# Performance work log

Hardware: AMD Instinct MI355X
Metric: run time of the kernel (lower is better)

The kernel has to match this reference:

```python
import jax, jax.numpy as jnp
import numpy as np

V, E, U, B, T = 50000, 256, 512, 256, 256  # vocab, embed, units, batch, seq_len


def setup_inputs() -> dict:
    key = jax.random.key(0)
    ks = jax.random.split(key, 10)
    tokens = jax.random.randint(ks[0], (B, T), 0, V)
    emb = jax.random.normal(ks[1], (V, E), dtype=jnp.float32) * 0.02
    s_e = 1.0 / np.sqrt(E)
    s_u = 1.0 / np.sqrt(U)
    W0 = jax.random.normal(ks[2], (E, 4 * U), dtype=jnp.float32) * s_e
    U0 = jax.random.normal(ks[3], (U, 4 * U), dtype=jnp.float32) * s_u
    b0 = jnp.zeros((4 * U,), dtype=jnp.float32)
    W1 = jax.random.normal(ks[4], (U, 4 * U), dtype=jnp.float32) * s_u
    U1 = jax.random.normal(ks[5], (U, 4 * U), dtype=jnp.float32) * s_u
    b1 = jnp.zeros((4 * U,), dtype=jnp.float32)
    Wd = jax.random.normal(ks[6], (U, 1), dtype=jnp.float32) * s_u
    bd = jnp.zeros((1,), dtype=jnp.float32)
    return {"tokens": tokens, "emb": emb, "W0": W0, "U0": U0, "b0": b0,
            "W1": W1, "U1": U1, "b1": b1, "Wd": Wd, "bd": bd}


def _lstm_gates(z, c):
    # Keras gate order: i, f, g (candidate), o
    i, f, g, o = jnp.split(z, 4, axis=-1)
    c_new = jax.nn.sigmoid(f) * c + jax.nn.sigmoid(i) * jnp.tanh(g)
    h_new = jax.nn.sigmoid(o) * jnp.tanh(c_new)
    return h_new, c_new


def reference(tokens, emb, W0, U0, b0, W1, U1, b1, Wd, bd):
    x = emb[tokens]  # [B, T, E]
    # Precompute input projections for layer 0 in one big GEMM: [T, B, 4U]
    xz0 = jnp.einsum('bte,ef->tbf', x, W0) + b0

    h0 = jnp.zeros((tokens.shape[0], U0.shape[0]), dtype=x.dtype)
    c0 = jnp.zeros_like(h0)
    h1 = jnp.zeros_like(h0)
    c1 = jnp.zeros_like(h0)

    def step(carry, xz_t):
        h0, c0, h1, c1 = carry
        h0, c0 = _lstm_gates(xz_t + h0 @ U0, c0)
        h1, c1 = _lstm_gates(h0 @ W1 + h1 @ U1 + b1, c1)
        return (h0, c0, h1, c1), None

    (h0, c0, h1, c1), _ = jax.lax.scan(step, (h0, c0, h1, c1), xz0)
    return jax.nn.sigmoid(h1 @ Wd + bd)  # [B, 1]
```

## Files before the change

### kernel.cpp

```cpp
#include <hip/hip_runtime.h>
#include <hip/hip_bf16.h>
#include <math.h>

#define VB 50000
#define EE 256
#define UU 512
#define BB 256
#define TT 256
#define G4 2048

typedef __attribute__((ext_vector_type(8))) short short8;
typedef __attribute__((ext_vector_type(2))) unsigned long long u64x2;
typedef __attribute__((ext_vector_type(4))) float f32x4;

__device__ __forceinline__ float sigf(float x){ return 1.0f/(1.0f+expf(-x)); }
__device__ __forceinline__ unsigned short f2bf(float f){
    __hip_bfloat16 h = __float2bfloat16(f);
    unsigned short s; __builtin_memcpy(&s,&h,2); return s;
}
__device__ __forceinline__ float bf2f(unsigned short u){
    unsigned int x = ((unsigned int)u)<<16; float f; __builtin_memcpy(&f,&x,4); return f;
}

__device__ __forceinline__ unsigned int cldu(const unsigned int* p){
    return __hip_atomic_load(p, __ATOMIC_RELAXED, __HIP_MEMORY_SCOPE_AGENT);
}
__device__ __forceinline__ void cstu(unsigned int* p, unsigned int v){
    __hip_atomic_store(p, v, __ATOMIC_RELAXED, __HIP_MEMORY_SCOPE_AGENT);
}

__device__ __forceinline__ short8 cld16w(const unsigned short* p){
    short8 v;
    asm volatile("global_load_dwordx4 %0, %1, off sc1"
                 : "=&v"(v) : "v"(p));
    return v;
}
__device__ __forceinline__ void cst16w(unsigned long long* dp, u64x2 v){
    asm volatile("global_store_dwordx4 %0, %1, off sc1"
                 :: "v"(dp), "v"(v) : "memory");
}

__global__ __launch_bounds__(256) void wtrans(const float* __restrict__ in, int rows,
                                              unsigned short* __restrict__ out,
                                              int Kout, int koff) {
    __shared__ float tl[32][33];
    int tx = threadIdx.x, ty = threadIdx.y;
    int c0 = blockIdx.x * 32, k0 = blockIdx.y * 32;
    #pragma unroll
    for (int i = 0; i < 4; i++)
        tl[ty + i * 8][tx] = in[(size_t)(k0 + ty + i * 8) * G4 + c0 + tx];
    __syncthreads();
    #pragma unroll
    for (int i = 0; i < 4; i++)
        out[(size_t)(c0 + ty + i * 8) * Kout + koff + k0 + tx] = f2bf(tl[tx][ty + i * 8]);
}

__global__ __launch_bounds__(64) void xgather(const int* __restrict__ tokens,
                                              const float* __restrict__ emb,
                                              unsigned short* __restrict__ xbf) {
    int flat = blockIdx.x;
    int b = flat & 255, t = flat >> 8;
    int tok = tokens[b * TT + t];
    float4 v = ((const float4*)(emb + (size_t)tok * EE))[threadIdx.x];
    ushort4 o;
    o.x = f2bf(v.x); o.y = f2bf(v.y); o.z = f2bf(v.z); o.w = f2bf(v.w);
    ((ushort4*)(xbf + ((size_t)t * BB + b) * EE))[threadIdx.x] = o;
}

__global__ __launch_bounds__(256, 1) void rnn_persist(
    const unsigned short* __restrict__ Wt0,
    const unsigned short* __restrict__ Wt1,
    const unsigned short* __restrict__ xbf,
    const int* __restrict__ tokens, const float* __restrict__ emb,
    const float* __restrict__ b0v, const float* __restrict__ b1v,
    unsigned short* __restrict__ h0buf,
    unsigned short* __restrict__ h1buf,
    unsigned int* __restrict__ bars,
    int use_xbf)
{
    extern __shared__ char smem[];
    unsigned short* wl  = (unsigned short*)smem;
    unsigned short* hst = (unsigned short*)(smem + 131072);
    int*            tokl = (int*)(smem + 131072 + 3072);

    const int tid   = threadIdx.x;
    const int bid   = blockIdx.x;
    const int g     = bid >> 6;
    const int local = bid & 63;
    const int layer = local >> 5;
    const int u0    = (local & 31) * 16;
    const int row0  = g * 64;
    const int K     = layer ? 1024 : 768;
    const int KT    = K / 32;
    const unsigned short* Wt = layer ? Wt1 : Wt0;
    const float* bR = layer ? b1v : b0v;

    const int nch = 4 * KT * 64;
    for (int i = tid; i < nch; i += 256) {
        int n  = i & 15;
        int q2 = (i >> 4) & 3;
        int t2 = i >> 6;
        int kt = t2 % KT, gate = t2 / KT;
        const unsigned short* src = Wt + (size_t)(gate * UU + u0 + n) * K + kt * 32 + q2 * 8;
        *(short8*)(wl + (size_t)i * 8) = *(const short8*)src;
    }

    float gb[4];
    #pragma unroll
    for (int gate = 0; gate < 4; gate++) gb[gate] = bR[gate * UU + u0 + (tid & 15)];
    float cst[4] = {0.f, 0.f, 0.f, 0.f};

    const int lane = tid & 63;
    const int w    = tid >> 6;
    const int n16  = lane & 15;
    const int q    = lane >> 4;
    const int q8   = q * 8;
    const int myrow = row0 + w * 16 + n16;
    const unsigned short* wlane = wl + lane * 8;

    unsigned int* flg = bars + (size_t)g * 1024;
    unsigned int* myFlag = flg + local;
    const unsigned int* pollp = flg + lane;
    const int pollSlack = (layer == 0 && lane >= 32) ? 6 : 0;

    const size_t HS = (size_t)BB * UU;

    __syncthreads();

    for (int p = 0; p <= TT; p++) {
        const bool active = layer ? (p >= 1) : (p < TT);

        f32x4 acc[4];
        #pragma unroll
        for (int gate = 0; gate < 4; gate++)
            acc[gate] = (f32x4){gb[gate], gb[gate], gb[gate], gb[gate]};

        short8 xv[8];
        if (layer == 0 && p < TT) {
            if (!use_xbf) {
                if (tid < 64) tokl[tid] = tokens[(size_t)(row0 + tid) * TT + p];
                __syncthreads();
                const float* ep = emb + (size_t)tokl[w * 16 + n16] * EE + q8;
                #pragma unroll
                for (int kt = 0; kt < 8; kt++) {
                    float4 f0 = *(const float4*)(ep + kt * 32);
                    float4 f1 = *(const float4*)(ep + kt * 32 + 4);
                    union { unsigned short s[8]; short8 v; } u;
                    u.s[0]=f2bf(f0.x); u.s[1]=f2bf(f0.y); u.s[2]=f2bf(f0.z); u.s[3]=f2bf(f0.w);
                    u.s[4]=f2bf(f1.x); u.s[5]=f2bf(f1.y); u.s[6]=f2bf(f1.z); u.s[7]=f2bf(f1.w);
                    #pragma unroll
                    for (int gate = 0; gate < 4; gate++) {
                        short8 bv = *(const short8*)(wlane + (size_t)(gate * KT + kt) * 512);
                        acc[gate] = __builtin_amdgcn_mfma_f32_16x16x32_bf16(u.v, bv, acc[gate], 0, 0, 0);
                    }
                }
            } else {
                const unsigned short* xp = xbf + ((size_t)p * BB + myrow) * EE + q8;
                #pragma unroll
                for (int kt = 0; kt < 8; kt++)
                    xv[kt] = *(const short8*)(xp + kt * 32);
            }
        }

        if (layer == 0) {
            if (p < TT) {
                if (tid < 64) {
                    const int thr = p - pollSlack;
                    for (;;) {
                        bool bad = ((int)cldu(pollp) < thr);
                        if (__ballot(bad) == 0ULL) break;
                        __builtin_amdgcn_s_sleep(1);
                    }
                }
                __syncthreads();

                const unsigned short* h0r = h0buf + (size_t)(p & 7) * HS;
                unsigned short* hw = h0buf + (size_t)((p + 1) & 7) * HS;
                const unsigned short* ah = h0r + (size_t)myrow * UU + q8;
                short8 hb[16];
                #pragma unroll
                for (int i = 0; i < 16; i++) hb[i] = cld16w(ah + i * 32);
                if (use_xbf) {
                    #pragma unroll
                    for (int kt = 0; kt < 8; kt++) {
                        #pragma unroll
                        for (int gate = 0; gate < 4; gate++) {
                            short8 bv = *(const short8*)(wlane + (size_t)(gate * KT + kt) * 512);
                            acc[gate] = __builtin_amdgcn_mfma_f32_16x16x32_bf16(xv[kt], bv, acc[gate], 0, 0, 0);
                        }
                    }
                }
                asm volatile("s_waitcnt vmcnt(0)" ::: "memory");
                __builtin_amdgcn_sched_barrier(0);
                #pragma unroll
                for (int i = 0; i < 16; i++) {
                    #pragma unroll
                    for (int gate = 0; gate < 4; gate++) {
                        short8 bv = *(const short8*)(wlane + (size_t)(gate * KT + 8 + i) * 512);
                        acc[gate] = __builtin_amdgcn_mfma_f32_16x16x32_bf16(hb[i], bv, acc[gate], 0, 0, 0);
                    }
                }

                #pragma unroll
                for (int r = 0; r < 4; r++) {
                    float zi = acc[0][r];
                    float zf = acc[1][r];
                    float zg = acc[2][r];
                    float zo = acc[3][r];
                    float cn = sigf(zf) * cst[r] + sigf(zi) * tanhf(zg);
                    cst[r] = cn;
                    hst[(w * 16 + q * 4 + r) * 24 + n16] = f2bf(sigf(zo) * tanhf(cn));
                }
                __syncthreads();
                if (tid < 128) {
                    int row = tid >> 1, half = tid & 1;
                    u64x2 sv = *(const u64x2*)(hst + row * 24 + half * 8);
                    unsigned long long* dp = (unsigned long long*)
                        (hw + (size_t)(row0 + row) * UU + u0 + half * 8);
                    cst16w(dp, sv);
                }
            }
        } else {
            if (active) {
                const unsigned short* h0r = h0buf + (size_t)(p & 7) * HS;
                const unsigned short* h1r = h1buf + (size_t)((p + 1) & 1) * HS;
                unsigned short* hw = h1buf + (size_t)(p & 1) * HS;
                const unsigned short* a0 = h0r + (size_t)myrow * UU + q8;
                const unsigned short* a1 = h1r + (size_t)myrow * UU + q8;

                for (;;) {
                    bool bad = (lane < 32) && ((int)cldu(pollp) < p);
                    if (__ballot(bad) == 0ULL) break;
                    __builtin_amdgcn_s_sleep(1);
                }
                short8 ha[16];
                #pragma unroll
                for (int i = 0; i < 16; i++) ha[i] = cld16w(a0 + i * 32);

                for (;;) {
                    bool bad = (lane >= 32) && ((int)cldu(pollp) < p);
                    if (__ballot(bad) == 0ULL) break;
                    __builtin_amdgcn_s_sleep(1);
                }
                short8 hc[16];
                #pragma unroll
                for (int i = 0; i < 16; i++) hc[i] = cld16w(a1 + i * 32);

                asm volatile("s_waitcnt vmcnt(16)" ::: "memory");
                __builtin_amdgcn_sched_barrier(0);
                #pragma unroll
                for (int i = 0; i < 16; i++) {
                    #pragma unroll
                    for (int gate = 0; gate < 4; gate++) {
                        short8 bv = *(const short8*)(wlane + (size_t)(gate * KT + i) * 512);
                        acc[gate] = __builtin_amdgcn_mfma_f32_16x16x32_bf16(ha[i], bv, acc[gate], 0, 0, 0);
                    }
                }
                asm volatile("s_waitcnt vmcnt(0)" ::: "memory");
                __builtin_amdgcn_sched_barrier(0);
                #pragma unroll
                for (int i = 0; i < 16; i++) {
                    #pragma unroll
                    for (int gate = 0; gate < 4; gate++) {
                        short8 bv = *(const short8*)(wlane + (size_t)(gate * KT + 16 + i) * 512);
                        acc[gate] = __builtin_amdgcn_mfma_f32_16x16x32_bf16(hc[i], bv, acc[gate], 0, 0, 0);
                    }
                }

                #pragma unroll
                for (int r = 0; r < 4; r++) {
                    float zi = acc[0][r];
                    float zf = acc[1][r];
                    float zg = acc[2][r];
                    float zo = acc[3][r];
                    float cn = sigf(zf) * cst[r] + sigf(zi) * tanhf(zg);
                    cst[r] = cn;
                    hst[(w * 16 + q * 4 + r) * 24 + n16] = f2bf(sigf(zo) * tanhf(cn));
                }
                __syncthreads();
                if (tid < 128) {
                    int row = tid >> 1, half = tid & 1;
                    u64x2 sv = *(const u64x2*)(hst + row * 24 + half * 8);
                    unsigned long long* dp = (unsigned long long*)
                        (hw + (size_t)(row0 + row) * UU + u0 + half * 8);
                    cst16w(dp, sv);
                }
            }
        }

        if (p < TT) {
            asm volatile("s_waitcnt vmcnt(0)" ::: "memory");
            __syncthreads();
            if (tid == 0) cstu(myFlag, (unsigned int)(p + 1));
        }
    }
}

__global__ __launch_bounds__(64) void dense_out(
    const unsigned short* __restrict__ h, const float* __restrict__ Wd,
    const float* __restrict__ bd, float* __restrict__ out)
{
    int b = blockIdx.x;
    int lane = threadIdx.x;
    float s = 0.f;
    #pragma unroll
    for (int k = lane; k < UU; k += 64) s += bf2f(h[(size_t)b * UU + k]) * Wd[k];
    #pragma unroll
    for (int off = 32; off > 0; off >>= 1) s += __shfl_down(s, off);
    if (lane == 0) out[b] = sigf(s + bd[0]);
}

extern "C" void kernel_launch(void* const* d_in, const int* in_sizes, int n_in,
                              void* d_out, int out_size, void* d_ws, size_t ws_size,
                              hipStream_t stream) {
    const int*   tokens = (const int*)  d_in[0];
    const float* emb    = (const float*)d_in[1];
    const float* W0     = (const float*)d_in[2];
    const float* U0     = (const float*)d_in[3];
    const float* b0     = (const float*)d_in[4];
    const float* W1     = (const float*)d_in[5];
    const float* U1     = (const float*)d_in[6];
    const float* b1     = (const float*)d_in[7];
    const float* Wd     = (const float*)d_in[8];
    const float* bd     = (const float*)d_in[9];
    float* out = (float*)d_out;

    const size_t oWt0 = 0;
    const size_t oWt1 = (size_t)G4 * 768 * 2;
    const size_t oH0  = oWt1 + (size_t)G4 * 1024 * 2;
    const size_t oH1  = oH0 + (size_t)8 * BB * UU * 2;
    const size_t oBar = oH1 + (size_t)2 * BB * UU * 2;
    const size_t oX   = oBar + 32768;
    const size_t needFull = oX + (size_t)TT * BB * EE * 2;
    int use_xbf = (ws_size >= needFull) ? 1 : 0;

    unsigned short* Wt0p = (unsigned short*)((char*)d_ws + oWt0);
    unsigned short* Wt1p = (unsigned short*)((char*)d_ws + oWt1);
    unsigned short* h0p  = (unsigned short*)((char*)d_ws + oH0);
    unsigned short* h1p  = (unsigned short*)((char*)d_ws + oH1);
    unsigned int*   barp = (unsigned int*)  ((char*)d_ws + oBar);
    unsigned short* xbfp = (unsigned short*)((char*)d_ws + oX);

    hipMemsetAsync((char*)d_ws + oH0, 0, oX - oH0, stream);

    wtrans<<<dim3(G4 / 32, EE / 32), dim3(32, 8), 0, stream>>>(W0, EE, Wt0p, 768, 0);
    wtrans<<<dim3(G4 / 32, UU / 32), dim3(32, 8), 0, stream>>>(U0, UU, Wt0p, 768, 256);
    wtrans<<<dim3(G4 / 32, UU / 32), dim3(32, 8), 0, stream>>>(W1, UU, Wt1p, 1024, 0);
    wtrans<<<dim3(G4 / 32, UU / 32), dim3(32, 8), 0, stream>>>(U1, UU, Wt1p, 1024, 512);

    if (use_xbf)
        xgather<<<dim3(BB * TT), dim3(64), 0, stream>>>(tokens, emb, xbfp);

    {
        const size_t shmem = 131072 + 3072 + 256;
        hipFuncSetAttribute((const void*)rnn_persist,
                            hipFuncAttributeMaxDynamicSharedMemorySize, (int)shmem);
        void* args[] = {(void*)&Wt0p, (void*)&Wt1p, (void*)&xbfp,
                        (void*)&tokens, (void*)&emb, (void*)&b0, (void*)&b1,
                        (void*)&h0p, (void*)&h1p, (void*)&barp, (void*)&use_xbf};
        hipLaunchCooperativeKernel((const void*)rnn_persist, dim3(256), dim3(256),
                                   args, shmem, stream);
    }

    dense_out<<<dim3(BB), dim3(64), 0, stream>>>(h1p, Wd, bd, out);
}
```

Before: 1.978 ms.

## Deepen hidden-state ring buffers and replace sc1 loads with periodic acquire fences

Grows the h0 and h1 ring buffers to 16 slots each. Hidden-state loads now go through the normal cached path instead of sc1, and an agent-scope acquire fence every 8 steps is meant to invalidate stale cached copies. The layer-0 wait on layer-1 progress moves from before the compute to just before the h0 store, so the compute overlaps that wait. Only slot 0 and the flag area are zeroed now, not the whole buffer region. The scheme depends on the 16-slot ring being deep enough that a reused slot's cached lines are never read stale between fences, which is a subtle correctness risk.

```diff
diff --git a/kernel.cpp b/kernel.cpp
--- a/kernel.cpp
+++ b/kernel.cpp
@@ -29,9 +29,9 @@
     __hip_atomic_store(p, v, __ATOMIC_RELAXED, __HIP_MEMORY_SCOPE_AGENT);
 }
 
-__device__ __forceinline__ short8 cld16w(const unsigned short* p){
+__device__ __forceinline__ short8 cld16c(const unsigned short* p){
     short8 v;
-    asm volatile("global_load_dwordx4 %0, %1, off sc1"
+    asm volatile("global_load_dwordx4 %0, %1, off"
                  : "=&v"(v) : "v"(p));
     return v;
 }
@@ -121,14 +121,14 @@
     unsigned int* flg = bars + (size_t)g * 1024;
     unsigned int* myFlag = flg + local;
     const unsigned int* pollp = flg + lane;
-    const int pollSlack = (layer == 0 && lane >= 32) ? 6 : 0;
 
     const size_t HS = (size_t)BB * UU;
 
     __syncthreads();
 
     for (int p = 0; p <= TT; p++) {
-        const bool active = layer ? (p >= 1) : (p < TT);
+        if ((p & 7) == 0)
+            __builtin_amdgcn_fence(__ATOMIC_ACQUIRE, "agent");
 
         f32x4 acc[4];
         #pragma unroll
@@ -165,21 +165,20 @@
         if (layer == 0) {
             if (p < TT) {
                 if (tid < 64) {
-                    const int thr = p - pollSlack;
                     for (;;) {
-                        bool bad = ((int)cldu(pollp) < thr);
+                        bool bad = (lane < 32) && ((int)cldu(pollp) < p);
                         if (__ballot(bad) == 0ULL) break;
                         __builtin_amdgcn_s_sleep(1);
                     }
                 }
                 __syncthreads();
 
-                const unsigned short* h0r = h0buf + (size_t)(p & 7) * HS;
-                unsigned short* hw = h0buf + (size_t)((p + 1) & 7) * HS;
+                const unsigned short* h0r = h0buf + (size_t)(p & 15) * HS;
+                unsigned short* hw = h0buf + (size_t)((p + 1) & 15) * HS;
                 const unsigned short* ah = h0r + (size_t)myrow * UU + q8;
                 short8 hb[16];
                 #pragma unroll
-                for (int i = 0; i < 16; i++) hb[i] = cld16w(ah + i * 32);
+                for (int i = 0; i < 16; i++) hb[i] = cld16c(ah + i * 32);
                 if (use_xbf) {
                     #pragma unroll
                     for (int kt = 0; kt < 8; kt++) {
@@ -212,6 +211,17 @@
                     hst[(w * 16 + q * 4 + r) * 24 + n16] = f2bf(sigf(zo) * tanhf(cn));
                 }
                 __syncthreads();
+
+                {
+                    const int thr = p - 6;
+                    if (thr > 0) {
+                        for (;;) {
+                            bool bad = (lane >= 32) && ((int)cldu(pollp) < thr);
+                            if (__ballot(bad) == 0ULL) break;
+                            __builtin_amdgcn_s_sleep(1);
+                        }
+                    }
+                }
                 if (tid < 128) {
                     int row = tid >> 1, half = tid & 1;
                     u64x2 sv = *(const u64x2*)(hst + row * 24 + half * 8);
@@ -221,10 +231,10 @@
                 }
             }
         } else {
-            if (active) {
-                const unsigned short* h0r = h0buf + (size_t)(p & 7) * HS;
-                const unsigned short* h1r = h1buf + (size_t)((p + 1) & 1) * HS;
-                unsigned short* hw = h1buf + (size_t)(p & 1) * HS;
+            if (p >= 1) {
+                const unsigned short* h0r = h0buf + (size_t)(p & 15) * HS;
+                const unsigned short* h1r = h1buf + (size_t)((p - 1) & 15) * HS;
+                unsigned short* hw = h1buf + (size_t)(p & 15) * HS;
                 const unsigned short* a0 = h0r + (size_t)myrow * UU + q8;
                 const unsigned short* a1 = h1r + (size_t)myrow * UU + q8;
 
@@ -235,7 +245,7 @@
                 }
                 short8 ha[16];
                 #pragma unroll
-                for (int i = 0; i < 16; i++) ha[i] = cld16w(a0 + i * 32);
+                for (int i = 0; i < 16; i++) ha[i] = cld16c(a0 + i * 32);
 
                 for (;;) {
                     bool bad = (lane >= 32) && ((int)cldu(pollp) < p);
@@ -244,7 +254,7 @@
                 }
                 short8 hc[16];
                 #pragma unroll
-                for (int i = 0; i < 16; i++) hc[i] = cld16w(a1 + i * 32);
+                for (int i = 0; i < 16; i++) hc[i] = cld16c(a1 + i * 32);
 
                 asm volatile("s_waitcnt vmcnt(16)" ::: "memory");
                 __builtin_amdgcn_sched_barrier(0);
@@ -325,11 +335,12 @@
     const float* bd     = (const float*)d_in[9];
     float* out = (float*)d_out;
 
+    const size_t SLOT = (size_t)BB * UU * 2;
     const size_t oWt0 = 0;
     const size_t oWt1 = (size_t)G4 * 768 * 2;
     const size_t oH0  = oWt1 + (size_t)G4 * 1024 * 2;
-    const size_t oH1  = oH0 + (size_t)8 * BB * UU * 2;
-    const size_t oBar = oH1 + (size_t)2 * BB * UU * 2;
+    const size_t oH1  = oH0 + 16 * SLOT;
+    const size_t oBar = oH1 + 16 * SLOT;
     const size_t oX   = oBar + 32768;
     const size_t needFull = oX + (size_t)TT * BB * EE * 2;
     int use_xbf = (ws_size >= needFull) ? 1 : 0;
@@ -341,7 +352,9 @@
     unsigned int*   barp = (unsigned int*)  ((char*)d_ws + oBar);
     unsigned short* xbfp = (unsigned short*)((char*)d_ws + oX);
 
-    hipMemsetAsync((char*)d_ws + oH0, 0, oX - oH0, stream);
+    hipMemsetAsync(h0p, 0, SLOT, stream);
+    hipMemsetAsync(h1p, 0, SLOT, stream);
+    hipMemsetAsync(barp, 0, 32768, stream);
 
     wtrans<<<dim3(G4 / 32, EE / 32), dim3(32, 8), 0, stream>>>(W0, EE, Wt0p, 768, 0);
     wtrans<<<dim3(G4 / 32, UU / 32), dim3(32, 8), 0, stream>>>(U0, UU, Wt0p, 768, 256);
```

Result: no change. 1.980 ms (+0.1%).
